# Kernel tuning notes

Hardware: AMD Instinct MI355X
Metric: run time of the kernel (lower is better)

Reference implementation:

```python
import jax, jax.numpy as jnp
import numpy as np

INPUT_SIZE = 128
OUTPUT_SIZE = 32
NUM_BASIS = 256


def setup_inputs() -> dict:
    key = jax.random.key(0)
    k_x, k_w, k_c = jax.random.split(key, 3)
    x = jax.random.normal(k_x, (INPUT_SIZE,), dtype=jnp.float32)
    weights = jax.random.normal(k_w, (OUTPUT_SIZE, NUM_BASIS), dtype=jnp.float32)
    centers = jax.random.normal(k_c, (NUM_BASIS, OUTPUT_SIZE, INPUT_SIZE), dtype=jnp.float32)
    # Lambda_inv initialized as identity repeated, per the torch module
    Lambda_inv = jnp.broadcast_to(
        jnp.eye(INPUT_SIZE, dtype=jnp.float32),
        (NUM_BASIS, OUTPUT_SIZE, INPUT_SIZE, INPUT_SIZE),
    ).copy()
    # bnds = tensor(bounds).T -> shape (2, output_size); bounds are (-1, 1) pairs
    bnds = jnp.stack([
        -jnp.ones((OUTPUT_SIZE,), dtype=jnp.float32),
        jnp.ones((OUTPUT_SIZE,), dtype=jnp.float32),
    ])
    return {"x": x, "weights": weights, "centers": centers,
            "Lambda_inv": Lambda_inv, "bnds": bnds}


def reference(x, weights, centers, Lambda_inv, bnds):
    # diff: (B, O, I) — broadcast x against all basis/output centers at once
    diff = x[None, None, :] - centers
    # batched quadratic form diff^T Lambda_inv diff -> (B, O); replaces the
    # num_basis x output_size Python double loop with one fused einsum
    quad = jnp.einsum('boi,boij,boj->bo', diff, Lambda_inv, diff)
    rbf_values = jnp.exp(-0.5 * quad)  # (B, O)
    # matmul(weights, rbf_values).diag() == sum_b weights[o,b] * rbf_values[b,o]
    policy = jnp.einsum('ob,bo->o', weights, rbf_values)  # (O,)
    policy = jnp.tanh(policy)
    return (policy + 1.0) * 0.5 * (bnds[1] - bnds[0]) + bnds[0]
```

## Files before the change

kernel.cpp:

```cpp
#include <hip/hip_runtime.h>

#define NB 256
#define NO 32
#define NI 128

__global__ __launch_bounds__(256, 8) void rbf_quad_kernel(
    const float* __restrict__ x,
    const float* __restrict__ centers,
    const float* __restrict__ Lam,
    float* __restrict__ rbf)
{
    __shared__ float diff_lds[4][NI];
    const int lane = threadIdx.x & 63;
    const int wid  = threadIdx.x >> 6;
    const int p    = blockIdx.x * 4 + wid;

    const float2 xv = *(const float2*)(x + 2 * lane);
    const float2 cv = *(const float2*)(centers + (size_t)p * NI + 2 * lane);
    *(float2*)(&diff_lds[wid][2 * lane]) = make_float2(xv.x - cv.x, xv.y - cv.y);
    __syncthreads();

    const int c = 4 * (lane & 31);
    const int h = lane >> 5;
    const float4 dj = *(const float4*)(&diff_lds[wid][c]);

    const float4* __restrict__ Lrow = (const float4*)(Lam + (size_t)p * (NI * NI));
    float acc = 0.0f;
    #pragma unroll 8
    for (int it = 0; it < NI / 2; ++it) {
        const float4 L  = Lrow[(size_t)it * 64 + lane];
        const float  di = diff_lds[wid][2 * it + h];
        acc = fmaf(di,
                   fmaf(L.x, dj.x, fmaf(L.y, dj.y, fmaf(L.z, dj.z, L.w * dj.w))),
                   acc);
    }

    #pragma unroll
    for (int off = 32; off; off >>= 1) acc += __shfl_xor(acc, off);

    if (lane == 0) rbf[p] = expf(-0.5f * acc);
}

__global__ __launch_bounds__(256) void rbf_policy_kernel(
    const float* __restrict__ weights,
    const float* __restrict__ rbf,
    const float* __restrict__ bnds,
    float* __restrict__ out)
{
    const int o = blockIdx.x;
    const int t = threadIdx.x;

    float v = weights[o * NB + t] * rbf[t * NO + o];

    #pragma unroll
    for (int off = 32; off; off >>= 1) v += __shfl_xor(v, off);

    __shared__ float part[4];
    if ((t & 63) == 0) part[t >> 6] = v;
    __syncthreads();

    if (t == 0) {
        const float s   = part[0] + part[1] + part[2] + part[3];
        const float pol = tanhf(s);
        const float lo  = bnds[o];
        const float hi  = bnds[NO + o];
        out[o] = (pol + 1.0f) * 0.5f * (hi - lo) + lo;
    }
}

extern "C" void kernel_launch(void* const* d_in, const int* in_sizes, int n_in,
                              void* d_out, int out_size, void* d_ws, size_t ws_size,
                              hipStream_t stream) {
    const float* x       = (const float*)d_in[0];
    const float* weights = (const float*)d_in[1];
    const float* centers = (const float*)d_in[2];
    const float* Lam     = (const float*)d_in[3];
    const float* bnds    = (const float*)d_in[4];
    float* out = (float*)d_out;
    float* rbf = (float*)d_ws;

    rbf_quad_kernel<<<2048, 256, 0, stream>>>(x, centers, Lam, rbf);
    rbf_policy_kernel<<<NO, NB, 0, stream>>>(weights, rbf, bnds, out);
}
```

Baseline: 101.9 us.

## Spread each quad-form across the whole block with unrolled nontemporal loads

Each block of 256 threads now works through its four (basis, output) pairs one after another, instead of giving one pair to each wave. Every thread issues 16 fully unrolled float4 loads per pair into four independent accumulators, which puts more independent loads in flight. The Lambda_inv stream is read with nontemporal loads to avoid polluting the cache. Partial sums from the four waves are combined through LDS, which adds an extra barrier and a small cross-wave reduction.

After: 270.2 us. 2.65x slower.

```diff
diff --git a/kernel.cpp b/kernel.cpp
--- a/kernel.cpp
+++ b/kernel.cpp
@@ -3,6 +3,12 @@
 #define NB 256
 #define NO 32
 #define NI 128
+
+typedef float f32x4 __attribute__((ext_vector_type(4)));
+
+__device__ __forceinline__ float dot4(f32x4 a, f32x4 b) {
+    return fmaf(a.x, b.x, fmaf(a.y, b.y, fmaf(a.z, b.z, a.w * b.w)));
+}
 
 __global__ __launch_bounds__(256, 8) void rbf_quad_kernel(
     const float* __restrict__ x,
@@ -11,34 +17,56 @@
     float* __restrict__ rbf)
 {
     __shared__ float diff_lds[4][NI];
-    const int lane = threadIdx.x & 63;
-    const int wid  = threadIdx.x >> 6;
-    const int p    = blockIdx.x * 4 + wid;
+    __shared__ float part[4][4];
+    const int t    = threadIdx.x;
+    const int lane = t & 63;
+    const int wid  = t >> 6;
+    const int p0   = blockIdx.x * 4;
 
     const float2 xv = *(const float2*)(x + 2 * lane);
-    const float2 cv = *(const float2*)(centers + (size_t)p * NI + 2 * lane);
+    const float2 cv = *(const float2*)(centers + (size_t)(p0 + wid) * NI + 2 * lane);
     *(float2*)(&diff_lds[wid][2 * lane]) = make_float2(xv.x - cv.x, xv.y - cv.y);
     __syncthreads();
 
-    const int c = 4 * (lane & 31);
-    const int h = lane >> 5;
-    const float4 dj = *(const float4*)(&diff_lds[wid][c]);
+    const int c4    = t & 31;
+    const int rbase = t >> 5;
 
-    const float4* __restrict__ Lrow = (const float4*)(Lam + (size_t)p * (NI * NI));
-    float acc = 0.0f;
-    #pragma unroll 8
-    for (int it = 0; it < NI / 2; ++it) {
-        const float4 L  = Lrow[(size_t)it * 64 + lane];
-        const float  di = diff_lds[wid][2 * it + h];
-        acc = fmaf(di,
-                   fmaf(L.x, dj.x, fmaf(L.y, dj.y, fmaf(L.z, dj.z, L.w * dj.w))),
-                   acc);
+    float acc[4];
+
+    #pragma unroll
+    for (int q = 0; q < 4; ++q) {
+        const f32x4 dj = *(const f32x4*)(&diff_lds[q][4 * c4]);
+        const f32x4* __restrict__ Lq =
+            (const f32x4*)(Lam + (size_t)(p0 + q) * (NI * NI));
+        const float* dl = diff_lds[q];
+        float a0 = 0.0f, a1 = 0.0f, a2 = 0.0f, a3 = 0.0f;
+        #pragma unroll
+        for (int s = 0; s < 16; s += 4) {
+            const f32x4 L0 = __builtin_nontemporal_load(Lq + (s + 0) * 256 + t);
+            const f32x4 L1 = __builtin_nontemporal_load(Lq + (s + 1) * 256 + t);
+            const f32x4 L2 = __builtin_nontemporal_load(Lq + (s + 2) * 256 + t);
+            const f32x4 L3 = __builtin_nontemporal_load(Lq + (s + 3) * 256 + t);
+            a0 = fmaf(dl[(s + 0) * 8 + rbase], dot4(L0, dj), a0);
+            a1 = fmaf(dl[(s + 1) * 8 + rbase], dot4(L1, dj), a1);
+            a2 = fmaf(dl[(s + 2) * 8 + rbase], dot4(L2, dj), a2);
+            a3 = fmaf(dl[(s + 3) * 8 + rbase], dot4(L3, dj), a3);
+        }
+        acc[q] = (a0 + a1) + (a2 + a3);
     }
 
     #pragma unroll
-    for (int off = 32; off; off >>= 1) acc += __shfl_xor(acc, off);
+    for (int q = 0; q < 4; ++q) {
+        float v = acc[q];
+        #pragma unroll
+        for (int off = 32; off; off >>= 1) v += __shfl_xor(v, off);
+        if (lane == 0) part[wid][q] = v;
+    }
+    __syncthreads();
 
-    if (lane == 0) rbf[p] = expf(-0.5f * acc);
+    if (t < 4) {
+        const float s_ = part[0][t] + part[1][t] + part[2][t] + part[3][t];
+        rbf[p0 + t] = expf(-0.5f * s_);
+    }
 }
 
 __global__ __launch_bounds__(256) void rbf_policy_kernel(
```
